# Kernel optimization log

Measured on AMD Instinct MI355X. Metric: run time of the kernel, lower is better.

Reference implementation:

```python
import jax, jax.numpy as jnp
import numpy as np

N, C, H, W = 8, 64, 56, 56
NL_C = 0.5
EPS = 1e-5


def _bn(x, gamma, beta, mean, var):
    # eval-mode BatchNorm2d over channel dim of NCHW
    inv = jax.lax.rsqrt(var + EPS)
    return (x - mean[:, None, None]) * (inv * gamma)[:, None, None] + beta[:, None, None]


def setup_inputs() -> dict:
    key = jax.random.key(0)
    ks = jax.random.split(key, 11)
    l = jax.random.normal(ks[0], (N, C, H, W), jnp.float32)
    w_inside = jax.random.normal(ks[1], (C, C, 1, 1), jnp.float32) * 0.1  # 1x1 conv, OIHW
    gamma1 = jax.random.normal(ks[2], (C,), jnp.float32)
    beta1 = jax.random.normal(ks[3], (C,), jnp.float32)
    mean1 = jax.random.normal(ks[4], (C,), jnp.float32)
    var1 = jax.random.uniform(ks[5], (C,), jnp.float32, 0.5, 1.5)
    w_dw = jax.random.normal(ks[6], (C, 1, 3, 3), jnp.float32) * 0.1  # depthwise 3x3
    gamma2 = jax.random.normal(ks[7], (C,), jnp.float32)
    beta2 = jax.random.normal(ks[8], (C,), jnp.float32)
    mean2 = jax.random.normal(ks[9], (C,), jnp.float32)
    var2 = jax.random.uniform(ks[10], (C,), jnp.float32, 0.5, 1.5)
    return dict(l=l, w_inside=w_inside, gamma1=gamma1, beta1=beta1, mean1=mean1,
                var1=var1, w_dw=w_dw, gamma2=gamma2, beta2=beta2, mean2=mean2, var2=var2)


def reference(l, w_inside, gamma1, beta1, mean1, var1, w_dw, gamma2, beta2, mean2, var2):
    n, n_in, h, w = l.shape
    c_red = int(NL_C * n_in)  # channels used for theta/phi

    # conv_inside: 1x1 conv (no bias) + BN + relu6 -> g
    g = jax.lax.conv_general_dilated(l, w_inside, (1, 1), 'VALID',
                                     dimension_numbers=('NCHW', 'OIHW', 'NCHW'))
    g = jnp.clip(_bn(g, gamma1, beta1, mean1, var1), 0.0, 6.0)

    theta = l[:, :c_red]  # == phi in the original code
    # f: [N, H, W, H, W]
    f = jnp.einsum('niab,nicd->nabcd', theta, theta)
    # softmax over flattened (a,b) then over flattened (c,d)
    f = jax.nn.softmax(f.reshape(n, h * w, h, w), axis=1)
    f = jax.nn.softmax(f.reshape(n, h * w, h * w), axis=2)
    f = f.reshape(n, h, w, h, w)

    out = jnp.einsum('nabcd,nicd->niab', f, g)
    out = out / h * w  # (f / H) * W as in the original

    # depthwise 3x3 conv, pad 1, no bias
    out = jax.lax.conv_general_dilated(out, w_dw, (1, 1), ((1, 1), (1, 1)),
                                       dimension_numbers=('NCHW', 'OIHW', 'NCHW'),
                                       feature_group_count=n_in)
    out = _bn(out, gamma2, beta2, mean2, var2)
    return out + l
```

## Files before the change

### kernel.cpp

```cpp
#include <hip/hip_runtime.h>

#define HW   3136
#define NCH  64
#define CRED 32
#define NB   8
#define EPSV 1e-5f
#define QS2  7

#define SQRT_L2E 1.2011224087f
#define LOG2_L2E 0.5287663729f

typedef __attribute__((ext_vector_type(8))) short short8;
typedef __attribute__((ext_vector_type(4))) float f32x4;
typedef __attribute__((ext_vector_type(2))) float f32x2;
typedef _Float16 half_t;
typedef __attribute__((ext_vector_type(2))) _Float16 half2v;
typedef __attribute__((ext_vector_type(4))) _Float16 half4v;

#define MFMA_B16 __builtin_amdgcn_mfma_f32_16x16x32_bf16

__device__ __forceinline__ unsigned short f2b(float x) {
    union { float f; unsigned u; } v; v.f = x;
    unsigned r = v.u + 0x7fff + ((v.u >> 16) & 1);
    return (unsigned short)(r >> 16);
}

__device__ __forceinline__ float ex2(float x) {
#if __has_builtin(__builtin_amdgcn_exp2f)
    return __builtin_amdgcn_exp2f(x);
#else
    float r;
    asm volatile("v_exp_f32 %0, %1" : "=v"(r) : "v"(x));
    return r;
#endif
}

__device__ __forceinline__ unsigned cvtpk(float a, float b) {
    unsigned r;
    asm("v_cvt_pk_bf16_f32 %0, %1, %2" : "=v"(r) : "v"(a), "v"(b));
    return r;
}

__device__ __forceinline__ void gload_lds16(const void* g, void* l) {
    __builtin_amdgcn_global_load_lds(
        (const __attribute__((address_space(1))) void*)g,
        (__attribute__((address_space(3))) void*)l, 16, 0, 0);
}

__global__ __launch_bounds__(256) void k1_conv1x1(
    const float* __restrict__ l, const float* __restrict__ w,
    const float* __restrict__ gamma, const float* __restrict__ beta,
    const float* __restrict__ mean, const float* __restrict__ var,
    unsigned short* __restrict__ theta_bf, unsigned short* __restrict__ Gbt)
{
    __shared__ float Wt[NCH][65];
    __shared__ float Lt[NCH][65];
    const int t  = threadIdx.x;
    const int n  = blockIdx.y;
    const int p0 = blockIdx.x * 64;

    for (int idx = t; idx < NCH * 64; idx += 256) {
        int c = idx >> 6, j = idx & 63;
        Wt[c][j] = w[j * NCH + c];
        Lt[c][j] = l[((size_t)n * NCH + c) * HW + p0 + j];
    }
    __syncthreads();

    {
        const int p = t >> 2, c0 = (t & 3) * 8;
        unsigned short pk[8];
#pragma unroll
        for (int j = 0; j < 8; ++j) pk[j] = f2b(Lt[c0 + j][p] * SQRT_L2E);
        *(short8*)&theta_bf[((size_t)n * HW + p0 + p) * CRED + c0] = *(short8*)pk;
    }

    const int i   = t & 63;
    const int pj0 = t >> 6;
    const float mu = mean[i];
    const float sc = rsqrtf(var[i] + EPSV) * gamma[i];
    const float bi = beta[i];

    float acc[16];
#pragma unroll
    for (int k = 0; k < 16; ++k) acc[k] = 0.f;
#pragma unroll
    for (int c = 0; c < NCH; ++c) {
        float wci = Wt[c][i];
#pragma unroll
        for (int k = 0; k < 16; ++k) acc[k] += wci * Lt[c][pj0 + 4 * k];
    }
    __syncthreads();

#pragma unroll
    for (int k = 0; k < 16; ++k) {
        float y = (acc[k] - mu) * sc + bi;
        y = fminf(fmaxf(y, 0.f), 6.f);
        Wt[i][pj0 + 4 * k] = y;
    }
    __syncthreads();

    {
        const int ir = t >> 2, pc = (t & 3) * 16;
        unsigned short pk[16];
#pragma unroll
        for (int j = 0; j < 16; ++j) pk[j] = f2b(Wt[ir][pc + j]);
        unsigned short* dst = &Gbt[((size_t)n * NCH + ir) * HW + p0 + pc];
        *(short8*)&dst[0] = *(short8*)&pk[0];
        *(short8*)&dst[8] = *(short8*)&pk[8];
    }
}

__global__ __launch_bounds__(256) void k2s_stats(
    const unsigned short* __restrict__ theta_bf, float* __restrict__ zpart)
{
    const int t = threadIdx.x, w = t >> 6, lane = t & 63;
    const int lo = lane & 15, hi = lane >> 4;
    const int n = blockIdx.z, psp = blockIdx.y;
    const int q0 = blockIdx.x * 64;

    const unsigned short* thn = theta_bf + (size_t)n * HW * CRED;

    const short8 afrag = *(const short8*)&thn[(q0 + w * 16 + lo) * CRED + hi * 8];

    float z[4] = {0.f, 0.f, 0.f, 0.f};

    short8 bf[4];
    {
        const int p0 = psp * 448;
#pragma unroll
        for (int ss = 0; ss < 4; ++ss)
            bf[ss] = *(const short8*)&thn[(p0 + ss * 16 + lo) * CRED + hi * 8];
    }

    for (int pt = 0; pt < 7; ++pt) {
        const int pn = psp * 448 + ((pt < 6) ? (pt + 1) * 64 : 6 * 64);
        short8 nf[4];
#pragma unroll
        for (int ss = 0; ss < 4; ++ss)
            nf[ss] = *(const short8*)&thn[(pn + ss * 16 + lo) * CRED + hi * 8];

#pragma unroll
        for (int ss = 0; ss < 4; ++ss) {
            f32x4 zero = {0.f, 0.f, 0.f, 0.f};
            f32x4 d = MFMA_B16(afrag, bf[ss], zero, 0, 0, 0);
#pragma unroll
            for (int r = 0; r < 4; ++r) z[r] += ex2(d[r]);
        }

#pragma unroll
        for (int ss = 0; ss < 4; ++ss) bf[ss] = nf[ss];
    }

#pragma unroll
    for (int r = 0; r < 4; ++r) {
        float v = z[r];
        v += __shfl_xor(v, 1, 64);
        v += __shfl_xor(v, 2, 64);
        v += __shfl_xor(v, 4, 64);
        v += __shfl_xor(v, 8, 64);
        z[r] = v;
    }
    if (lo == 0) {
        f32x4 st = {z[0], z[1], z[2], z[3]};
        *(f32x4*)&zpart[((size_t)psp * NB + n) * HW + q0 + w * 16 + hi * 4] = st;
    }
}

__global__ __launch_bounds__(256) void k2c_combine(
    const float* __restrict__ zpart, float* __restrict__ crow)
{
    const int idx = blockIdx.x * 256 + threadIdx.x;
    float s = 0.f;
#pragma unroll
    for (int ps = 0; ps < QS2; ++ps) s += zpart[(size_t)ps * NB * HW + idx];
    crow[idx] = LOG2_L2E - __log2f(s);
}

__global__ __launch_bounds__(256) void k3f_fused(
    const unsigned short* __restrict__ theta_bf,
    const unsigned short* __restrict__ Gbt,
    const float* __restrict__ crow,
    half_t* __restrict__ Part, float* __restrict__ Zpart)
{
    __shared__ unsigned short Glt[64][64];
    __shared__ unsigned short El[64][76];

    const int t = threadIdx.x, w = t >> 6, lane = t & 63;
    const int lo = lane & 15, hi = lane >> 4;
    const int n = blockIdx.z, qsp = blockIdx.y;
    const int pblk = blockIdx.x * 64;
    const int pw = w * 16;

    const unsigned short* thn = theta_bf + (size_t)n * HW * CRED;
    const float* crn = crow + (size_t)n * HW;
    const unsigned short* gbn = Gbt + (size_t)n * NCH * HW;

    const short8 bp = *(const short8*)&thn[(pblk + pw + lo) * CRED + hi * 8];

    const int s0 = (w * 2 + 0) * 64 + lane;
    const int s1 = (w * 2 + 1) * 64 + lane;
    const int r0 = s0 >> 3, j0 = (s0 & 7) ^ (r0 & 7);
    const int r1 = s1 >> 3, j1 = (s1 & 7) ^ (r1 & 7);
    char* lbase = (char*)&Glt[0][0];

    f32x4 acc[4];
#pragma unroll
    for (int it = 0; it < 4; ++it) acc[it] = (f32x4){0.f, 0.f, 0.f, 0.f};
    float zl = 0.f;

    for (int tile = 0; tile < 7; ++tile) {
        const int qb = qsp * 448 + tile * 64;
        __syncthreads();
        gload_lds16(&gbn[(size_t)r0 * HW + qb + j0 * 8],
                    lbase + (size_t)(w * 2 + 0) * 1024);
        gload_lds16(&gbn[(size_t)r1 * HW + qb + j1 * 8],
                    lbase + (size_t)(w * 2 + 1) * 1024);
        short8 aqr[4];
        f32x4  cvr[4];
#pragma unroll
        for (int s = 0; s < 4; ++s) {
            aqr[s] = *(const short8*)&thn[(qb + s * 16 + lo) * CRED + hi * 8];
            cvr[s] = *(const f32x4*)&crn[qb + s * 16 + hi * 4];
        }
        __syncthreads();

#pragma unroll
        for (int s = 0; s < 4; ++s) {
            f32x4 d = MFMA_B16(aqr[s], bp, cvr[s], 0, 0, 0);
            float e0 = ex2(ex2(d[0]));
            float e1 = ex2(ex2(d[1]));
            float e2 = ex2(ex2(d[2]));
            float e3 = ex2(ex2(d[3]));
            zl += (e0 + e1) + (e2 + e3);
            unsigned* dst = (unsigned*)&El[pw + lo][s * 16 + hi * 4];
            dst[0] = cvtpk(e0, e1);
            dst[1] = cvtpk(e2, e3);
        }

        const unsigned short* gl = &Glt[0][0];
#pragma unroll
        for (int ks = 0; ks < 2; ++ks) {
            const short8 ae = *(const short8*)&El[pw + lo][ks * 32 + hi * 8];
#pragma unroll
            for (int it = 0; it < 4; ++it) {
                const int row = it * 16 + lo;
                const int cc  = (ks * 4 + hi) ^ (row & 7);
                const short8 bg = *(const short8*)&gl[row * 64 + cc * 8];
                acc[it] = MFMA_B16(ae, bg, acc[it], 0, 0, 0);
            }
        }
    }

    half_t* Pn = Part + ((size_t)n * QS2 + qsp) * (size_t)NCH * HW;
#pragma unroll
    for (int it = 0; it < 4; ++it) {
        half4v h;
        h[0] = (half_t)acc[it][0]; h[1] = (half_t)acc[it][1];
        h[2] = (half_t)acc[it][2]; h[3] = (half_t)acc[it][3];
        *(half4v*)&Pn[(size_t)(it * 16 + lo) * HW + pblk + pw + hi * 4] = h;
    }
    zl += __shfl_xor(zl, 16, 64);
    zl += __shfl_xor(zl, 32, 64);
    if (lane < 16)
        Zpart[((size_t)n * QS2 + qsp) * HW + pblk + pw + lane] = zl;
}

__global__ __launch_bounds__(256) void k34_reduce_dw(
    const half_t* __restrict__ Part, const float* __restrict__ Zpart,
    const float* __restrict__ l, const float* __restrict__ wdw,
    const float* __restrict__ gamma, const float* __restrict__ beta,
    const float* __restrict__ mean, const float* __restrict__ var,
    float* __restrict__ out)
{
    __shared__ float op[4][16][56];
    __shared__ float zsh[16][56];
    __shared__ float wsh[36];

    const int t    = threadIdx.x;
    const int band = blockIdx.x;
    const int i0   = blockIdx.y * 4;
    const int n    = blockIdx.z;
    const int y0   = band * 14;

    if (t < 36) wsh[t] = wdw[i0 * 9 + t];

    if (t < 16 * 14) {
        const int row = t / 14, xq = (t % 14) * 4;
        const int yy = y0 - 1 + row;
        if (yy >= 0 && yy < 56) {
            const int p = yy * 56 + xq;
            f32x4 z = {0.f, 0.f, 0.f, 0.f};
#pragma unroll
            for (int qs = 0; qs < QS2; ++qs)
                z += *(const f32x4*)&Zpart[((size_t)n * QS2 + qs) * HW + p];
            f32x4 zi = {1.f / z[0], 1.f / z[1], 1.f / z[2], 1.f / z[3]};
            *(f32x4*)&zsh[row][xq] = zi;
        }
    }
    __syncthreads();

    for (int idx = t; idx < 4 * 16 * 14; idx += 256) {
        const int c = idx / (16 * 14), rem = idx % (16 * 14);
        const int row = rem / 14, xq = (rem % 14) * 4;
        const int yy = y0 - 1 + row;
        if (yy >= 0 && yy < 56) {
            const int p = yy * 56 + xq;
            const int i = i0 + c;
            f32x4 s = {0.f, 0.f, 0.f, 0.f};
#pragma unroll
            for (int qs = 0; qs < QS2; ++qs) {
                half4v h = *(const half4v*)
                    &Part[(((size_t)n * QS2 + qs) * NCH + i) * HW + p];
                s[0] += (float)h[0]; s[1] += (float)h[1];
                s[2] += (float)h[2]; s[3] += (float)h[3];
            }
            const f32x4 zi = *(const f32x4*)&zsh[row][xq];
            f32x4 o = {s[0] * zi[0], s[1] * zi[1], s[2] * zi[2], s[3] * zi[3]};
            *(f32x4*)&op[c][row][xq] = o;
        }
    }
    __syncthreads();

    for (int idx = t; idx < 4 * 14 * 14; idx += 256) {
        const int c = idx / (14 * 14), rem = idx % (14 * 14);
        const int y = y0 + rem / 14, xq = (rem % 14) * 4;
        const int i = i0 + c;

        float res[4];
#pragma unroll
        for (int j = 0; j < 4; ++j) {
            const int x = xq + j;
            float acc = 0.f;
#pragma unroll
            for (int dy = -1; dy <= 1; ++dy) {
                const int yy = y + dy;
                if (yy < 0 || yy >= 56) continue;
                const int ly = yy - (y0 - 1);
#pragma unroll
                for (int dx = -1; dx <= 1; ++dx) {
                    const int xx = x + dx;
                    if (xx < 0 || xx >= 56) continue;
                    acc += wsh[c * 9 + (dy + 1) * 3 + (dx + 1)] * op[c][ly][xx];
                }
            }
            res[j] = acc;
        }
        const float sc = rsqrtf(var[i] + EPSV) * gamma[i];
        const float mu = mean[i], bi = beta[i];
        const size_t e = ((size_t)n * NCH + i) * HW + y * 56 + xq;
        const f32x4 lv = *(const f32x4*)&l[e];
        f32x4 o = {(res[0] - mu) * sc + bi + lv[0],
                   (res[1] - mu) * sc + bi + lv[1],
                   (res[2] - mu) * sc + bi + lv[2],
                   (res[3] - mu) * sc + bi + lv[3]};
        *(f32x4*)&out[e] = o;
    }
}

extern "C" void kernel_launch(void* const* d_in, const int* in_sizes, int n_in,
                              void* d_out, int out_size, void* d_ws, size_t ws_size,
                              hipStream_t stream)
{
    const float* l      = (const float*)d_in[0];
    const float* w_in   = (const float*)d_in[1];
    const float* gamma1 = (const float*)d_in[2];
    const float* beta1  = (const float*)d_in[3];
    const float* mean1  = (const float*)d_in[4];
    const float* var1   = (const float*)d_in[5];
    const float* w_dw   = (const float*)d_in[6];
    const float* gamma2 = (const float*)d_in[7];
    const float* beta2  = (const float*)d_in[8];
    const float* mean2  = (const float*)d_in[9];
    const float* var2   = (const float*)d_in[10];
    float* out = (float*)d_out;

    char* ws = (char*)d_ws;
    const size_t szTheta = (size_t)NB * HW * CRED * 2;
    const size_t szGbt   = (size_t)NB * NCH * HW * 2;
    const size_t szCrow  = (size_t)NB * HW * 4;
    const size_t szZpt   = (size_t)QS2 * NB * HW * 4;
    const size_t szZp    = (size_t)NB * QS2 * HW * 4;

    unsigned short* theta_bf = (unsigned short*)ws;
    unsigned short* Gbt      = (unsigned short*)(ws + szTheta);
    float* crow   = (float*)(ws + szTheta + szGbt);
    float* zpart  = (float*)(ws + szTheta + szGbt + szCrow);
    float* Zp     = (float*)(ws + szTheta + szGbt + szCrow + szZpt);
    half_t* Part  = (half_t*)(ws + szTheta + szGbt + szCrow + szZpt + szZp);
    (void)ws_size;

    k1_conv1x1<<<dim3(HW / 64, NB), 256, 0, stream>>>(
        l, w_in, gamma1, beta1, mean1, var1, theta_bf, Gbt);

    k2s_stats<<<dim3(HW / 64, QS2, NB), 256, 0, stream>>>(theta_bf, zpart);

    k2c_combine<<<dim3((NB * HW) / 256), 256, 0, stream>>>(zpart, crow);

    k3f_fused<<<dim3(HW / 64, QS2, NB), 256, 0, stream>>>(
        theta_bf, Gbt, crow, Part, Zp);

    k34_reduce_dw<<<dim3(4, NCH / 4, NB), 256, 0, stream>>>(
        Part, Zp, l, w_dw, gamma2, beta2, mean2, var2, out);
}
```

Before: 95.84 us.

## Process two 64-row p-blocks per k3f block to reuse staged G tiles

Each k3f_fused block now handles two 64-wide p blocks (128 rows) instead of one. The G tile in LDS and the q-side theta and crow loads are reused across both. The grid's x dimension halves, with a has2 guard for the odd tail (HW/64 = 49 blocks). This cuts repeated global and LDS staging of G and the theta_q loads, but doubles accumulator registers per thread and roughly halves the block count. That may hurt occupancy and load balance, since the grid goes from 49x7x8 to 25x7x8 blocks.

```diff
diff --git a/kernel.cpp b/kernel.cpp
--- a/kernel.cpp
+++ b/kernel.cpp
@@ -16,6 +16,9 @@
 typedef _Float16 half_t;
 typedef __attribute__((ext_vector_type(2))) _Float16 half2v;
 typedef __attribute__((ext_vector_type(4))) _Float16 half4v;
+
+typedef short8 __attribute__((may_alias)) short8_ma;
+typedef unsigned __attribute__((may_alias)) uint_ma;
 
 #define MFMA_B16 __builtin_amdgcn_mfma_f32_16x16x32_bf16
 
@@ -176,6 +179,34 @@
     crow[idx] = LOG2_L2E - __log2f(s);
 }
 
+#define S_PV_GRP(BP, ACC, ZL)                                                  \
+    do {                                                                       \
+        _Pragma("unroll")                                                      \
+        for (int s = 0; s < 4; ++s) {                                          \
+            f32x4 d = MFMA_B16(aqr[s], BP, cvr[s], 0, 0, 0);                   \
+            float e0 = ex2(ex2(d[0]));                                         \
+            float e1 = ex2(ex2(d[1]));                                         \
+            float e2 = ex2(ex2(d[2]));                                         \
+            float e3 = ex2(ex2(d[3]));                                         \
+            ZL += (e0 + e1) + (e2 + e3);                                       \
+            uint_ma* dst = (uint_ma*)&El[pw + lo][s * 16 + hi * 4];            \
+            dst[0] = cvtpk(e0, e1);                                            \
+            dst[1] = cvtpk(e2, e3);                                            \
+        }                                                                      \
+        _Pragma("unroll")                                                      \
+        for (int ks = 0; ks < 2; ++ks) {                                       \
+            const short8 ae =                                                  \
+                *(const short8_ma*)&El[pw + lo][ks * 32 + hi * 8];             \
+            _Pragma("unroll")                                                  \
+            for (int it = 0; it < 4; ++it) {                                   \
+                const int row = it * 16 + lo;                                  \
+                const int cc  = (ks * 4 + hi) ^ (row & 7);                     \
+                const short8 bg = *(const short8_ma*)&gl[row * 64 + cc * 8];   \
+                ACC[it] = MFMA_B16(ae, bg, ACC[it], 0, 0, 0);                  \
+            }                                                                  \
+        }                                                                      \
+    } while (0)
+
 __global__ __launch_bounds__(256) void k3f_fused(
     const unsigned short* __restrict__ theta_bf,
     const unsigned short* __restrict__ Gbt,
@@ -188,25 +219,32 @@
     const int t = threadIdx.x, w = t >> 6, lane = t & 63;
     const int lo = lane & 15, hi = lane >> 4;
     const int n = blockIdx.z, qsp = blockIdx.y;
-    const int pblk = blockIdx.x * 64;
+    const int pblk = blockIdx.x * 128;
+    const bool has2 = (pblk + 128 <= HW);
+    const int pblk2 = has2 ? pblk + 64 : pblk;
     const int pw = w * 16;
 
     const unsigned short* thn = theta_bf + (size_t)n * HW * CRED;
     const float* crn = crow + (size_t)n * HW;
     const unsigned short* gbn = Gbt + (size_t)n * NCH * HW;
 
-    const short8 bp = *(const short8*)&thn[(pblk + pw + lo) * CRED + hi * 8];
+    const short8 bp0 = *(const short8*)&thn[(pblk  + pw + lo) * CRED + hi * 8];
+    const short8 bp1 = *(const short8*)&thn[(pblk2 + pw + lo) * CRED + hi * 8];
 
     const int s0 = (w * 2 + 0) * 64 + lane;
     const int s1 = (w * 2 + 1) * 64 + lane;
     const int r0 = s0 >> 3, j0 = (s0 & 7) ^ (r0 & 7);
     const int r1 = s1 >> 3, j1 = (s1 & 7) ^ (r1 & 7);
     char* lbase = (char*)&Glt[0][0];
-
-    f32x4 acc[4];
-#pragma unroll
-    for (int it = 0; it < 4; ++it) acc[it] = (f32x4){0.f, 0.f, 0.f, 0.f};
-    float zl = 0.f;
+    const unsigned short* gl = &Glt[0][0];
+
+    f32x4 accA[4], accB[4];
+#pragma unroll
+    for (int it = 0; it < 4; ++it) {
+        accA[it] = (f32x4){0.f, 0.f, 0.f, 0.f};
+        accB[it] = (f32x4){0.f, 0.f, 0.f, 0.f};
+    }
+    float zlA = 0.f, zlB = 0.f;
 
     for (int tile = 0; tile < 7; ++tile) {
         const int qb = qsp * 448 + tile * 64;
@@ -224,30 +262,10 @@
         }
         __syncthreads();
 
-#pragma unroll
-        for (int s = 0; s < 4; ++s) {
-            f32x4 d = MFMA_B16(aqr[s], bp, cvr[s], 0, 0, 0);
-            float e0 = ex2(ex2(d[0]));
-            float e1 = ex2(ex2(d[1]));
-            float e2 = ex2(ex2(d[2]));
-            float e3 = ex2(ex2(d[3]));
-            zl += (e0 + e1) + (e2 + e3);
-            unsigned* dst = (unsigned*)&El[pw + lo][s * 16 + hi * 4];
-            dst[0] = cvtpk(e0, e1);
-            dst[1] = cvtpk(e2, e3);
-        }
-
-        const unsigned short* gl = &Glt[0][0];
-#pragma unroll
-        for (int ks = 0; ks < 2; ++ks) {
-            const short8 ae = *(const short8*)&El[pw + lo][ks * 32 + hi * 8];
-#pragma unroll
-            for (int it = 0; it < 4; ++it) {
-                const int row = it * 16 + lo;
-                const int cc  = (ks * 4 + hi) ^ (row & 7);
-                const short8 bg = *(const short8*)&gl[row * 64 + cc * 8];
-                acc[it] = MFMA_B16(ae, bg, acc[it], 0, 0, 0);
-            }
+        S_PV_GRP(bp0, accA, zlA);
+        if (has2) {
+            __asm__ __volatile__("" ::: "memory");
+            S_PV_GRP(bp1, accB, zlB);
         }
     }
 
@@ -255,14 +273,28 @@
 #pragma unroll
     for (int it = 0; it < 4; ++it) {
         half4v h;
-        h[0] = (half_t)acc[it][0]; h[1] = (half_t)acc[it][1];
-        h[2] = (half_t)acc[it][2]; h[3] = (half_t)acc[it][3];
+        h[0] = (half_t)accA[it][0]; h[1] = (half_t)accA[it][1];
+        h[2] = (half_t)accA[it][2]; h[3] = (half_t)accA[it][3];
         *(half4v*)&Pn[(size_t)(it * 16 + lo) * HW + pblk + pw + hi * 4] = h;
     }
-    zl += __shfl_xor(zl, 16, 64);
-    zl += __shfl_xor(zl, 32, 64);
+    zlA += __shfl_xor(zlA, 16, 64);
+    zlA += __shfl_xor(zlA, 32, 64);
     if (lane < 16)
-        Zpart[((size_t)n * QS2 + qsp) * HW + pblk + pw + lane] = zl;
+        Zpart[((size_t)n * QS2 + qsp) * HW + pblk + pw + lane] = zlA;
+
+    if (has2) {
+#pragma unroll
+        for (int it = 0; it < 4; ++it) {
+            half4v h;
+            h[0] = (half_t)accB[it][0]; h[1] = (half_t)accB[it][1];
+            h[2] = (half_t)accB[it][2]; h[3] = (half_t)accB[it][3];
+            *(half4v*)&Pn[(size_t)(it * 16 + lo) * HW + pblk + 64 + pw + hi * 4] = h;
+        }
+        zlB += __shfl_xor(zlB, 16, 64);
+        zlB += __shfl_xor(zlB, 32, 64);
+        if (lane < 16)
+            Zpart[((size_t)n * QS2 + qsp) * HW + pblk + 64 + pw + lane] = zlB;
+    }
 }
 
 __global__ __launch_bounds__(256) void k34_reduce_dw(
@@ -396,7 +428,7 @@
 
     k2c_combine<<<dim3((NB * HW) / 256), 256, 0, stream>>>(zpart, crow);
 
-    k3f_fused<<<dim3(HW / 64, QS2, NB), 256, 0, stream>>>(
+    k3f_fused<<<dim3((HW + 127) / 128, QS2, NB), 256, 0, stream>>>(
         theta_bf, Gbt, crow, Part, Zp);
 
     k34_reduce_dw<<<dim3(4, NCH / 4, NB), 256, 0, stream>>>(
```

New measurement: 91.88 us. 4.1% less time.
